# Optimization experiments

Hardware: AMD Instinct MI355X
Metric: run time of the kernel (lower is better)

Reference implementation:

```python
import jax, jax.numpy as jnp
from jax import lax
import numpy as np

B, C, H, W = 4, 256, 64, 64
SPLIT = 8           # split_size
HEADS_BR = 4        # num_heads // 2 per branch
C2 = C // 2         # per-branch channels
HID = 4 * C         # mlp hidden
EPS = 1e-5


def layernorm(x, w, b):
    m = jnp.mean(x, -1, keepdims=True)
    v = jnp.mean((x - m) ** 2, -1, keepdims=True)
    return (x - m) * lax.rsqrt(v + EPS) * w + b


def lepe_attn(qk, v, gw, gb, Hsp, Wsp):
    # qk, v: (B, L, Cb) with L = H*W; windows of (Hsp, Wsp)
    Bq, L, Cb = qk.shape
    heads, hd = HEADS_BR, Cb // HEADS_BR
    nH, nW = H // Hsp, W // Wsp
    scale = hd ** -0.5
    # tokens -> windows -> heads: (B*nH*nW, heads, Hsp*Wsp, hd)
    qkw = (qk.reshape(Bq, nH, Hsp, nW, Wsp, Cb)
             .transpose(0, 1, 3, 2, 4, 5)
             .reshape(-1, Hsp * Wsp, heads, hd)
             .transpose(0, 2, 1, 3))
    # v as window images (B*nH*nW, Cb, Hsp, Wsp) for depthwise LePE conv
    vimg = (v.reshape(Bq, nH, Hsp, nW, Wsp, Cb)
              .transpose(0, 1, 3, 5, 2, 4)
              .reshape(-1, Cb, Hsp, Wsp))
    lepe = lax.conv_general_dilated(
        vimg, gw, (1, 1), 'SAME',
        dimension_numbers=('NCHW', 'OIHW', 'NCHW'),
        feature_group_count=Cb) + gb[None, :, None, None]
    vwin = vimg.reshape(-1, heads, hd, Hsp * Wsp).transpose(0, 1, 3, 2)
    lep = lepe.reshape(-1, heads, hd, Hsp * Wsp).transpose(0, 1, 3, 2)
    attn = jax.nn.softmax(
        jnp.einsum('whqd,whkd->whqk', qkw * scale, qkw), axis=-1)
    out = jnp.einsum('whqk,whkd->whqd', attn, vwin) + lep
    # windows -> image -> tokens
    out = (out.transpose(0, 2, 1, 3)
              .reshape(Bq, nH, nW, Hsp, Wsp, Cb)
              .transpose(0, 1, 3, 2, 4, 5)
              .reshape(Bq, L, Cb))
    return out


def setup_inputs() -> dict:
    key = jax.random.key(0)
    ks = jax.random.split(key, 8)
    p = lambda k, s: jax.random.normal(k, s, jnp.float32) * 0.02
    return {
        'x': jax.random.normal(ks[0], (B, C, H, W), jnp.float32),
        'norm1_w': jnp.ones((C,), jnp.float32),
        'norm1_b': jnp.zeros((C,), jnp.float32),
        'qkv_w': p(ks[1], (2 * C, C)),
        'getv_w0': p(ks[2], (C2, 1, 3, 3)),
        'getv_b0': jnp.zeros((C2,), jnp.float32),
        'getv_w1': p(ks[3], (C2, 1, 3, 3)),
        'getv_b1': jnp.zeros((C2,), jnp.float32),
        'proj_w': p(ks[4], (C, C)),
        'proj_b': jnp.zeros((C,), jnp.float32),
        'norm2_w': jnp.ones((C,), jnp.float32),
        'norm2_b': jnp.zeros((C,), jnp.float32),
        'fc1_w': p(ks[5], (HID, C)),
        'fc1_b': jnp.zeros((HID,), jnp.float32),
        'fc2_w': p(ks[6], (C, HID)),
        'fc2_b': jnp.zeros((C,), jnp.float32),
    }


def reference(x, norm1_w, norm1_b, qkv_w, getv_w0, getv_b0, getv_w1, getv_b1,
              proj_w, proj_b, norm2_w, norm2_b, fc1_w, fc1_b, fc2_w, fc2_b):
    b, c, h, w = x.shape
    x = x.reshape(b, c, h * w).transpose(0, 2, 1)        # (B, L, C)
    img = layernorm(x, norm1_w, norm1_b)
    qkv = img @ qkv_w.T                                  # (B, L, 2C)
    qk, v = qkv[..., :c], qkv[..., c:]                   # shared q=k, and v
    # branch 0: windows (H, split); branch 1: windows (split, W)
    x1 = lepe_attn(qk[..., :C2], v[..., :C2], getv_w0, getv_b0, h, SPLIT)
    x2 = lepe_attn(qk[..., C2:], v[..., C2:], getv_w1, getv_b1, SPLIT, w)
    att = jnp.concatenate([x1, x2], axis=2) @ proj_w.T + proj_b
    x = x + att
    y = layernorm(x, norm2_w, norm2_b)
    y = jax.nn.gelu(y @ fc1_w.T + fc1_b, approximate=False) @ fc2_w.T + fc2_b
    return x + y                                          # (B, L, C)
```

## Files before the change

### kernel.cpp

```cpp
#include <hip/hip_runtime.h>
#include <hip/hip_bf16.h>

#define BDIM 4
#define CDIM 256
#define HDIM 64
#define WDIM 64
#define LDIM 4096
#define ROWS 16384

typedef __attribute__((ext_vector_type(8))) short short8;
typedef __attribute__((ext_vector_type(4))) float f32x4;
typedef __attribute__((ext_vector_type(16))) float f32x16;
typedef unsigned int u32;

static __device__ __forceinline__ unsigned short f2bf(float f) {
    unsigned int x = __float_as_uint(f);
    unsigned int r = (x + 0x7fffu + ((x >> 16) & 1u)) >> 16;
    return (unsigned short)r;
}
static __device__ __forceinline__ float bf2f(unsigned int u) {
    return __uint_as_float(u << 16);
}
static __device__ __forceinline__ u32 pk2(float a, float b) {
    return (u32)f2bf(a) | ((u32)f2bf(b) << 16);
}

__global__ __launch_bounds__(256) void cvt4_kernel(
    const float* __restrict__ a, const float* __restrict__ b,
    const float* __restrict__ c, const float* __restrict__ d,
    unsigned short* __restrict__ oa, unsigned short* __restrict__ ob,
    unsigned short* __restrict__ oc, unsigned short* __restrict__ od)
{
    int i = blockIdx.x * 256 + threadIdx.x;
    const float* in; unsigned short* out; int off;
    if (i < 32768)       { in = a; out = oa; off = i; }
    else if (i < 49152)  { in = b; out = ob; off = i - 32768; }
    else if (i < 114688) { in = c; out = oc; off = i - 49152; }
    else if (i < 180224) { in = d; out = od; off = i - 114688; }
    else return;
    float4 f = reinterpret_cast<const float4*>(in)[off];
    reinterpret_cast<uint2*>(out)[off] = make_uint2(pk2(f.x, f.y), pk2(f.z, f.w));
}

__global__ __launch_bounds__(256) void norm_kernel(
    const float* __restrict__ xin,
    const float* __restrict__ w, const float* __restrict__ b,
    unsigned short* __restrict__ out,
    float* __restrict__ xT,
    int transposed_in)
{
    int wave = threadIdx.x >> 6;
    int lane = threadIdx.x & 63;
    int row = blockIdx.x * 4 + wave;
    float v[4];
    float sum = 0.f, sumsq = 0.f;
    if (transposed_in) {
        int bb = row >> 12;
        int l = row & 4095;
        const float* xb = xin + (size_t)bb * (CDIM * LDIM) + l;
        #pragma unroll
        for (int i = 0; i < 4; ++i) {
            int c = lane + i * 64;
            float t = xb[(size_t)c * LDIM];
            v[i] = t; sum += t; sumsq += t * t;
        }
    } else {
        const float* xr = xin + (size_t)row * CDIM;
        #pragma unroll
        for (int i = 0; i < 4; ++i) {
            float t = xr[lane + i * 64];
            v[i] = t; sum += t; sumsq += t * t;
        }
    }
    #pragma unroll
    for (int off = 32; off > 0; off >>= 1) {
        sum   += __shfl_xor(sum, off);
        sumsq += __shfl_xor(sumsq, off);
    }
    float mean = sum * (1.f / 256.f);
    float var  = sumsq * (1.f / 256.f) - mean * mean;
    float inv  = rsqrtf(var + 1e-5f);
    unsigned short* orow = out + (size_t)row * CDIM;
    #pragma unroll
    for (int i = 0; i < 4; ++i) {
        int c = lane + i * 64;
        if (xT) xT[(size_t)row * CDIM + c] = v[i];
        orow[c] = f2bf((v[i] - mean) * inv * w[c] + b[c]);
    }
}

__global__ __launch_bounds__(256) void mfma_gemm(
    const unsigned short* __restrict__ A,
    const unsigned short* __restrict__ Bm,
    const float* __restrict__ bias,
    const float* __restrict__ resid,
    void* __restrict__ outp,
    int N, int K, int mode)
{
    __shared__ unsigned short As[2][64 * 32];
    __shared__ unsigned short Bs[2][64 * 32];
    int tid  = threadIdx.x;
    int lane = tid & 63;
    int w    = tid >> 6;
    int wr   = w >> 1, wc = w & 1;
    int l15  = lane & 15, kbl = lane >> 4;

    int gx  = gridDim.x;
    int nwg = gx * gridDim.y;
    int bid = blockIdx.y * gx + blockIdx.x;
    int cpx = nwg >> 3;
    int swz = (bid & 7) * cpx + (bid >> 3);
    int n0 = (swz % gx) * 64;
    int m0 = (swz / gx) * 64;

    f32x4 acc[2][2];
    #pragma unroll
    for (int m = 0; m < 2; ++m)
        #pragma unroll
        for (int n = 0; n < 2; ++n)
            acc[m][n] = (f32x4){0.f, 0.f, 0.f, 0.f};

    int srow = tid >> 2;
    int sp   = tid & 3;
    int ss   = sp ^ (srow & 3);
    auto STAGE = [&](int buf, int k0) {
        const unsigned short* ga = A  + (size_t)(m0 + srow) * K + k0 + ss * 8;
        const unsigned short* gb = Bm + (size_t)(n0 + srow) * K + k0 + ss * 8;
        __builtin_amdgcn_global_load_lds(
            (const __attribute__((address_space(1))) void*)ga,
            (__attribute__((address_space(3))) void*)(As[buf] + tid * 8), 16, 0, 0);
        __builtin_amdgcn_global_load_lds(
            (const __attribute__((address_space(1))) void*)gb,
            (__attribute__((address_space(3))) void*)(Bs[buf] + tid * 8), 16, 0, 0);
    };

    STAGE(0, 0);
    __syncthreads();

    int cur = 0;
    for (int k0 = 0; k0 < K; k0 += 32) {
        if (k0 + 32 < K) STAGE(cur ^ 1, k0 + 32);

        short8 af[2], bf[2];
        #pragma unroll
        for (int m = 0; m < 2; ++m) {
            int row = wr * 32 + m * 16 + l15;
            af[m] = *reinterpret_cast<const short8*>(
                As[cur] + row * 32 + (kbl ^ (row & 3)) * 8);
        }
        #pragma unroll
        for (int n = 0; n < 2; ++n) {
            int row = wc * 32 + n * 16 + l15;
            bf[n] = *reinterpret_cast<const short8*>(
                Bs[cur] + row * 32 + (kbl ^ (row & 3)) * 8);
        }
        #pragma unroll
        for (int m = 0; m < 2; ++m)
            #pragma unroll
            for (int n = 0; n < 2; ++n)
                acc[m][n] = __builtin_amdgcn_mfma_f32_16x16x32_bf16(
                    af[m], bf[n], acc[m][n], 0, 0, 0);

        __syncthreads();
        cur ^= 1;
    }

    int r0 = kbl * 4;
    #pragma unroll
    for (int m = 0; m < 2; ++m) {
        #pragma unroll
        for (int n = 0; n < 2; ++n) {
            int col = n0 + wc * 32 + n * 16 + l15;
            #pragma unroll
            for (int r = 0; r < 4; ++r) {
                int row = m0 + wr * 32 + m * 16 + r0 + r;
                float v = acc[m][n][r];
                if (mode == 0) {
                    ((float*)outp)[(size_t)row * N + col] = v;
                } else if (mode == 1) {
                    ((unsigned short*)outp)[(size_t)row * N + col] = f2bf(v);
                } else if (mode == 2) {
                    v += bias[col];
                    v = 0.5f * v * (1.f + erff(v * 0.70710678118654752f));
                    ((unsigned short*)outp)[(size_t)row * N + col] = f2bf(v);
                } else {
                    v += bias[col] + resid[(size_t)row * N + col];
                    ((float*)outp)[(size_t)row * N + col] = v;
                }
            }
        }
    }
}

__global__ __launch_bounds__(512) void attn_kernel(
    const unsigned short* __restrict__ qkv,
    const float* __restrict__ gw0, const float* __restrict__ gb0,
    const float* __restrict__ gw1, const float* __restrict__ gb1,
    unsigned short* __restrict__ att)
{
    __shared__ unsigned short Kbuf[512 * 32];
    __shared__ unsigned short Vt[32 * 512];
    __shared__ float gwl[288];
    __shared__ float gbl[32];
    const int wh = blockIdx.x;
    const int br = wh >> 7, head = wh & 3, win = (wh >> 2) & 31;
    const int bb = win >> 3, wi = win & 7;
    const int tid = threadIdx.x;
    const int qk_off = br * 128 + head * 32;
    const int v_off = 256 + qk_off;
    const float sscale = 0.42044820762685725f;

    {
        const float* gw = br ? gw1 : gw0;
        const float* gb = br ? gb1 : gb0;
        if (tid < 288) gwl[tid] = gw[(head * 32) * 9 + tid];
        else if (tid >= 480) gbl[tid - 480] = gb[head * 32 + tid - 480];
    }
    {
        int t = tid;
        int l = (br == 0) ? ((t >> 3) * 64 + wi * 8 + (t & 7)) : (wi * 512 + t);
        const unsigned short* src = qkv + ((size_t)(bb * 4096 + l)) * 512 + qk_off;
        #pragma unroll
        for (int s = 0; s < 4; ++s) {
            uint4 raw = *reinterpret_cast<const uint4*>(src + s * 8);
            u32 rw[4] = {raw.x, raw.y, raw.z, raw.w};
            u32 ow[4];
            #pragma unroll
            for (int i = 0; i < 4; ++i) {
                float lo = bf2f(rw[i] & 0xffffu) * sscale;
                float hi = bf2f(rw[i] >> 16) * sscale;
                ow[i] = pk2(lo, hi);
            }
            int sl = s ^ ((t >> 1) & 3);
            *reinterpret_cast<uint4*>(Kbuf + t * 32 + sl * 8) =
                make_uint4(ow[0], ow[1], ow[2], ow[3]);
        }
    }
    {
        int kp = (tid & 255) * 2, dh = tid >> 8;
        int kq = kp + 1;
        int l0 = (br == 0) ? ((kp >> 3) * 64 + wi * 8 + (kp & 7)) : (wi * 512 + kp);
        int l1 = (br == 0) ? ((kq >> 3) * 64 + wi * 8 + (kq & 7)) : (wi * 512 + kq);
        const unsigned short* v0 = qkv + ((size_t)(bb * 4096 + l0)) * 512 + v_off + dh * 16;
        const unsigned short* v1 = qkv + ((size_t)(bb * 4096 + l1)) * 512 + v_off + dh * 16;
        uint4 a0 = *reinterpret_cast<const uint4*>(v0);
        uint4 a1 = *reinterpret_cast<const uint4*>(v0 + 8);
        uint4 b0 = *reinterpret_cast<const uint4*>(v1);
        uint4 b1 = *reinterpret_cast<const uint4*>(v1 + 8);
        u32 av[8] = {a0.x, a0.y, a0.z, a0.w, a1.x, a1.y, a1.z, a1.w};
        u32 bv[8] = {b0.x, b0.y, b0.z, b0.w, b1.x, b1.y, b1.z, b1.w};
        int slot = kp >> 3;
        #pragma unroll
        for (int dd = 0; dd < 16; ++dd) {
            u32 x0 = (dd & 1) ? (av[dd >> 1] >> 16) : (av[dd >> 1] & 0xffffu);
            u32 x1 = (dd & 1) ? (bv[dd >> 1] >> 16) : (bv[dd >> 1] & 0xffffu);
            int d = dh * 16 + dd;
            int sl = slot ^ (d & 7);
            *reinterpret_cast<u32*>(Vt + d * 512 + sl * 8 + (kp & 7)) = x0 | (x1 << 16);
        }
    }
    __syncthreads();

    const int lane = tid & 63;
    const int w = tid >> 6;
    const int ql = lane & 31;
    const int h = lane >> 5;
    const int q0 = w * 64;

    f32x16 O0, O1;
    #pragma unroll
    for (int i = 0; i < 16; ++i) { O0[i] = 0.f; O1[i] = 0.f; }
    float m0 = -1e30f, m1 = -1e30f, su0 = 0.f, su1 = 0.f;

    auto process = [&](int QS, f32x16& O, float& M, float& SU,
                       short8 kf0, short8 kf1, short8 vf0, short8 vf1) {
        int qrow = q0 + QS * 32 + ql;
        int sw = (qrow >> 1) & 3;
        short8 qf0 = *reinterpret_cast<const short8*>(Kbuf + qrow * 32 + ((0 + h) ^ sw) * 8);
        short8 qf1 = *reinterpret_cast<const short8*>(Kbuf + qrow * 32 + ((2 + h) ^ sw) * 8);
        f32x16 sacc;
        #pragma unroll
        for (int i = 0; i < 16; ++i) sacc[i] = 0.f;
        sacc = __builtin_amdgcn_mfma_f32_32x32x16_bf16(kf0, qf0, sacc, 0, 0, 0);
        sacc = __builtin_amdgcn_mfma_f32_32x32x16_bf16(kf1, qf1, sacc, 0, 0, 0);
        float mx = sacc[0];
        #pragma unroll
        for (int r = 1; r < 16; ++r) mx = fmaxf(mx, sacc[r]);
        mx = fmaxf(mx, __shfl_xor(mx, 32));
        float nm = fmaxf(M, mx);
        float fs = __expf(M - nm);
        M = nm;
        float p[16];
        float ps = 0.f;
        #pragma unroll
        for (int r = 0; r < 16; ++r) { p[r] = __expf(sacc[r] - nm); ps += p[r]; }
        ps += __shfl_xor(ps, 32);
        SU = SU * fs + ps;
        u32 P[8];
        #pragma unroll
        for (int g = 0; g < 4; ++g) {
            P[2 * g]     = pk2(p[4 * g],     p[4 * g + 1]);
            P[2 * g + 1] = pk2(p[4 * g + 2], p[4 * g + 3]);
        }
        u32 X[8];
        #pragma unroll
        for (int i = 0; i < 8; ++i) X[i] = __shfl_xor(P[i], 32);
        union { u32 u[4]; short8 s; } c0, c1;
        c0.u[0] = h ? X[2] : P[0];  c0.u[1] = h ? X[3] : P[1];
        c0.u[2] = h ? P[2] : X[0];  c0.u[3] = h ? P[3] : X[1];
        c1.u[0] = h ? X[6] : P[4];  c1.u[1] = h ? X[7] : P[5];
        c1.u[2] = h ? P[6] : X[4];  c1.u[3] = h ? P[7] : X[5];
        #pragma unroll
        for (int r = 0; r < 16; ++r) O[r] *= fs;
        O = __builtin_amdgcn_mfma_f32_32x32x16_bf16(vf0, c0.s, O, 0, 0, 0);
        O = __builtin_amdgcn_mfma_f32_32x32x16_bf16(vf1, c1.s, O, 0, 0, 0);
    };

    for (int kt = 0; kt < 16; ++kt) {
        int k0 = kt * 32;
        int krow = k0 + ql;
        int ksw = (krow >> 1) & 3;
        short8 kf0 = *reinterpret_cast<const short8*>(Kbuf + krow * 32 + ((0 + h) ^ ksw) * 8);
        short8 kf1 = *reinterpret_cast<const short8*>(Kbuf + krow * 32 + ((2 + h) ^ ksw) * 8);
        int ko0 = k0 + h * 8;
        int ko1 = k0 + 16 + h * 8;
        short8 vf0 = *reinterpret_cast<const short8*>(Vt + ql * 512 + ((ko0 >> 3) ^ (ql & 7)) * 8);
        short8 vf1 = *reinterpret_cast<const short8*>(Vt + ql * 512 + ((ko1 >> 3) ^ (ql & 7)) * 8);
        process(0, O0, m0, su0, kf0, kf1, vf0, vf1);
        process(1, O1, m1, su1, kf0, kf1, vf0, vf1);
    }

    #pragma unroll
    for (int QS = 0; QS < 2; ++QS) {
        f32x16& O = QS ? O1 : O0;
        float inv = 1.f / (QS ? su1 : su0);
        int qrow = q0 + QS * 32 + ql;
        int hs  = (br == 0) ? (qrow >> 3) : (qrow >> 6);
        int wsx = (br == 0) ? (qrow & 7)  : (qrow & 63);

        float lep[16];
        #pragma unroll
        for (int r = 0; r < 16; ++r) {
            int d = (r & 3) + 8 * (r >> 2) + 4 * h;
            lep[r] = gbl[d];
        }
        #pragma unroll
        for (int dy = -1; dy <= 1; ++dy) {
            int hn = hs + dy;
            bool okh = (br == 0) ? ((unsigned)hn < 64u) : ((unsigned)hn < 8u);
            #pragma unroll
            for (int dx = -1; dx <= 1; ++dx) {
                int wn = wsx + dx;
                bool okw = (br == 0) ? ((unsigned)wn < 8u) : ((unsigned)wn < 64u);
                if (okh && okw) {
                    int key = (br == 0) ? (hn * 8 + wn) : (hn * 64 + wn);
                    int t = (dy + 1) * 3 + (dx + 1);
                    #pragma unroll
                    for (int r = 0; r < 16; ++r) {
                        int d = (r & 3) + 8 * (r >> 2) + 4 * h;
                        float vv = bf2f((u32)(unsigned short)
                            Vt[d * 512 + (((key >> 3) ^ (d & 7)) * 8 + (key & 7))]);
                        lep[r] += vv * gwl[d * 9 + t];
                    }
                }
            }
        }

        int l = (br == 0) ? ((qrow >> 3) * 64 + wi * 8 + (qrow & 7)) : (wi * 512 + qrow);
        unsigned short* orow = att + ((size_t)(bb * 4096 + l)) * 256 + qk_off;
        #pragma unroll
        for (int g = 0; g < 4; ++g) {
            u32 lo = pk2(O[4 * g] * inv + lep[4 * g],
                         O[4 * g + 1] * inv + lep[4 * g + 1]);
            u32 hi = pk2(O[4 * g + 2] * inv + lep[4 * g + 2],
                         O[4 * g + 3] * inv + lep[4 * g + 3]);
            *reinterpret_cast<uint2*>(orow + 8 * g + 4 * h) = make_uint2(lo, hi);
        }
    }
}

extern "C" void kernel_launch(void* const* d_in, const int* in_sizes, int n_in,
                              void* d_out, int out_size, void* d_ws, size_t ws_size,
                              hipStream_t stream) {
    const float* x     = (const float*)d_in[0];
    const float* n1w   = (const float*)d_in[1];
    const float* n1b   = (const float*)d_in[2];
    const float* qkvw  = (const float*)d_in[3];
    const float* gw0   = (const float*)d_in[4];
    const float* gb0   = (const float*)d_in[5];
    const float* gw1   = (const float*)d_in[6];
    const float* gb1   = (const float*)d_in[7];
    const float* projw = (const float*)d_in[8];
    const float* projb = (const float*)d_in[9];
    const float* n2w   = (const float*)d_in[10];
    const float* n2b   = (const float*)d_in[11];
    const float* fc1w  = (const float*)d_in[12];
    const float* fc1b  = (const float*)d_in[13];
    const float* fc2w  = (const float*)d_in[14];
    const float* fc2b  = (const float*)d_in[15];
    float* out = (float*)d_out;
    char* wsb  = (char*)d_ws;

    float*          xT   = (float*)wsb;
    unsigned short* qkv  = (unsigned short*)(wsb + 16777216);
    unsigned short* att  = (unsigned short*)(wsb + 33554432);
    unsigned short* img  = (unsigned short*)(wsb + 41943040);
    unsigned short* wq   = (unsigned short*)(wsb + 50331648);
    unsigned short* wp   = (unsigned short*)(wsb + 50593792);
    unsigned short* w1   = (unsigned short*)(wsb + 50724864);
    unsigned short* w2   = (unsigned short*)(wsb + 51249152);
    unsigned short* ynorm  = img;
    unsigned short* hidden = (unsigned short*)wsb;

    cvt4_kernel<<<704, 256, 0, stream>>>(qkvw, projw, fc1w, fc2w, wq, wp, w1, w2);

    norm_kernel<<<4096, 256, 0, stream>>>(x, n1w, n1b, img, xT, 1);
    mfma_gemm<<<dim3(8, 256), 256, 0, stream>>>(img, wq, nullptr, nullptr, qkv, 512, 256, 1);
    attn_kernel<<<256, 512, 0, stream>>>(qkv, gw0, gb0, gw1, gb1, att);
    mfma_gemm<<<dim3(4, 256), 256, 0, stream>>>(att, wp, projb, xT, out, 256, 256, 3);
    norm_kernel<<<4096, 256, 0, stream>>>(out, n2w, n2b, ynorm, nullptr, 0);
    mfma_gemm<<<dim3(16, 256), 256, 0, stream>>>(ynorm, w1, fc1b, nullptr, hidden, 1024, 256, 2);
    mfma_gemm<<<dim3(4, 256), 256, 0, stream>>>(hidden, w2, fc2b, out, out, 256, 1024, 3);
}
```

Before: 162.4 us.

## Rework attention softmax: exp2 scaling, lazy rescale, permlane swap, hoisted Q fragments

```diff
diff --git a/kernel.cpp b/kernel.cpp
--- a/kernel.cpp
+++ b/kernel.cpp
@@ -23,6 +23,11 @@
 }
 static __device__ __forceinline__ u32 pk2(float a, float b) {
     return (u32)f2bf(a) | ((u32)f2bf(b) << 16);
+}
+static __device__ __forceinline__ u32 cvtpk(float lo, float hi) {
+    u32 r;
+    asm("v_cvt_pk_bf16_f32 %0, %1, %2" : "=v"(r) : "v"(lo), "v"(hi));
+    return r;
 }
 
 __global__ __launch_bounds__(256) void cvt4_kernel(
@@ -208,7 +213,7 @@
     const int tid = threadIdx.x;
     const int qk_off = br * 128 + head * 32;
     const int v_off = 256 + qk_off;
-    const float sscale = 0.42044820762685725f;
+    const float sscale = 0.50500977f;
 
     {
         const float* gw = br ? gw1 : gw0;
@@ -229,7 +234,7 @@
             for (int i = 0; i < 4; ++i) {
                 float lo = bf2f(rw[i] & 0xffffu) * sscale;
                 float hi = bf2f(rw[i] >> 16) * sscale;
-                ow[i] = pk2(lo, hi);
+                ow[i] = cvtpk(lo, hi);
             }
             int sl = s ^ ((t >> 1) & 3);
             *reinterpret_cast<uint4*>(Kbuf + t * 32 + sl * 8) =
@@ -267,53 +272,72 @@
     const int h = lane >> 5;
     const int q0 = w * 64;
 
+    short8 qA0, qA1, qB0, qB1;
+    {
+        int qrow = q0 + ql;
+        int sw = (qrow >> 1) & 3;
+        qA0 = *reinterpret_cast<const short8*>(Kbuf + qrow * 32 + ((0 + h) ^ sw) * 8);
+        qA1 = *reinterpret_cast<const short8*>(Kbuf + qrow * 32 + ((2 + h) ^ sw) * 8);
+        qrow = q0 + 32 + ql;
+        sw = (qrow >> 1) & 3;
+        qB0 = *reinterpret_cast<const short8*>(Kbuf + qrow * 32 + ((0 + h) ^ sw) * 8);
+        qB1 = *reinterpret_cast<const short8*>(Kbuf + qrow * 32 + ((2 + h) ^ sw) * 8);
+    }
+
     f32x16 O0, O1;
     #pragma unroll
     for (int i = 0; i < 16; ++i) { O0[i] = 0.f; O1[i] = 0.f; }
     float m0 = -1e30f, m1 = -1e30f, su0 = 0.f, su1 = 0.f;
 
-    auto process = [&](int QS, f32x16& O, float& M, float& SU,
+    auto process = [&](f32x16& O, float& M, float& SU,
+                       const short8& qf0, const short8& qf1,
                        short8 kf0, short8 kf1, short8 vf0, short8 vf1) {
-        int qrow = q0 + QS * 32 + ql;
-        int sw = (qrow >> 1) & 3;
-        short8 qf0 = *reinterpret_cast<const short8*>(Kbuf + qrow * 32 + ((0 + h) ^ sw) * 8);
-        short8 qf1 = *reinterpret_cast<const short8*>(Kbuf + qrow * 32 + ((2 + h) ^ sw) * 8);
         f32x16 sacc;
         #pragma unroll
         for (int i = 0; i < 16; ++i) sacc[i] = 0.f;
+        __builtin_amdgcn_s_setprio(1);
         sacc = __builtin_amdgcn_mfma_f32_32x32x16_bf16(kf0, qf0, sacc, 0, 0, 0);
         sacc = __builtin_amdgcn_mfma_f32_32x32x16_bf16(kf1, qf1, sacc, 0, 0, 0);
-        float mx = sacc[0];
-        #pragma unroll
-        for (int r = 1; r < 16; ++r) mx = fmaxf(mx, sacc[r]);
+        __builtin_amdgcn_s_setprio(0);
+        float t8[8];
+        #pragma unroll
+        for (int r = 0; r < 8; ++r) t8[r] = fmaxf(sacc[r], sacc[r + 8]);
+        float t4[4];
+        #pragma unroll
+        for (int r = 0; r < 4; ++r) t4[r] = fmaxf(t8[r], t8[r + 4]);
+        float mx = fmaxf(fmaxf(t4[0], t4[1]), fmaxf(t4[2], t4[3]));
         mx = fmaxf(mx, __shfl_xor(mx, 32));
-        float nm = fmaxf(M, mx);
-        float fs = __expf(M - nm);
-        M = nm;
+        bool defer = __all(mx <= M + 8.f);
+        float nm = defer ? M : fmaxf(M, mx);
         float p[16];
         float ps = 0.f;
         #pragma unroll
-        for (int r = 0; r < 16; ++r) { p[r] = __expf(sacc[r] - nm); ps += p[r]; }
+        for (int r = 0; r < 16; ++r) { p[r] = exp2f(sacc[r] - nm); ps += p[r]; }
         ps += __shfl_xor(ps, 32);
-        SU = SU * fs + ps;
-        u32 P[8];
-        #pragma unroll
-        for (int g = 0; g < 4; ++g) {
-            P[2 * g]     = pk2(p[4 * g],     p[4 * g + 1]);
-            P[2 * g + 1] = pk2(p[4 * g + 2], p[4 * g + 3]);
-        }
-        u32 X[8];
-        #pragma unroll
-        for (int i = 0; i < 8; ++i) X[i] = __shfl_xor(P[i], 32);
+        if (defer) {
+            SU += ps;
+        } else {
+            float fs = exp2f(M - nm);
+            SU = SU * fs + ps;
+            #pragma unroll
+            for (int r = 0; r < 16; ++r) O[r] *= fs;
+            M = nm;
+        }
+        u32 P0 = cvtpk(p[0],  p[1]),  P1 = cvtpk(p[2],  p[3]);
+        u32 P2 = cvtpk(p[4],  p[5]),  P3 = cvtpk(p[6],  p[7]);
+        u32 P4 = cvtpk(p[8],  p[9]),  P5 = cvtpk(p[10], p[11]);
+        u32 P6 = cvtpk(p[12], p[13]), P7 = cvtpk(p[14], p[15]);
+        asm volatile("v_permlane32_swap_b32 %0, %1" : "+v"(P0), "+v"(P2));
+        asm volatile("v_permlane32_swap_b32 %0, %1" : "+v"(P1), "+v"(P3));
+        asm volatile("v_permlane32_swap_b32 %0, %1" : "+v"(P4), "+v"(P6));
+        asm volatile("v_permlane32_swap_b32 %0, %1" : "+v"(P5), "+v"(P7));
         union { u32 u[4]; short8 s; } c0, c1;
-        c0.u[0] = h ? X[2] : P[0];  c0.u[1] = h ? X[3] : P[1];
-        c0.u[2] = h ? P[2] : X[0];  c0.u[3] = h ? P[3] : X[1];
-        c1.u[0] = h ? X[6] : P[4];  c1.u[1] = h ? X[7] : P[5];
-        c1.u[2] = h ? P[6] : X[4];  c1.u[3] = h ? P[7] : X[5];
-        #pragma unroll
-        for (int r = 0; r < 16; ++r) O[r] *= fs;
+        c0.u[0] = P0; c0.u[1] = P1; c0.u[2] = P2; c0.u[3] = P3;
+        c1.u[0] = P4; c1.u[1] = P5; c1.u[2] = P6; c1.u[3] = P7;
+        __builtin_amdgcn_s_setprio(1);
         O = __builtin_amdgcn_mfma_f32_32x32x16_bf16(vf0, c0.s, O, 0, 0, 0);
         O = __builtin_amdgcn_mfma_f32_32x32x16_bf16(vf1, c1.s, O, 0, 0, 0);
+        __builtin_amdgcn_s_setprio(0);
     };
 
     for (int kt = 0; kt < 16; ++kt) {
@@ -326,8 +350,8 @@
         int ko1 = k0 + 16 + h * 8;
         short8 vf0 = *reinterpret_cast<const short8*>(Vt + ql * 512 + ((ko0 >> 3) ^ (ql & 7)) * 8);
         short8 vf1 = *reinterpret_cast<const short8*>(Vt + ql * 512 + ((ko1 >> 3) ^ (ql & 7)) * 8);
-        process(0, O0, m0, su0, kf0, kf1, vf0, vf1);
-        process(1, O1, m1, su1, kf0, kf1, vf0, vf1);
+        process(O0, m0, su0, qA0, qA1, kf0, kf1, vf0, vf1);
+        process(O1, m1, su1, qB0, qB1, kf0, kf1, vf0, vf1);
     }
 
     #pragma unroll
```

Result: no change. 164.8 us (+1.5%).
